# Performance work log

Hardware: AMD Instinct MI355X
Metric: run time of the kernel (lower is better)

Reference implementation:

```python
import jax, jax.numpy as jnp
import numpy as np

N = 4096
CIN = 128
COUT = 128
J = 2
SLOPE = 0.2        # LeakyReLU negative slope (GAT-style)
NEG = -9.0e15      # mask fill value from the source
ATT = J * COUT     # att_slice


def _leaky(v):
    return jnp.where(v >= 0, v, SLOPE * v)


def setup_inputs() -> dict:
    key = jax.random.key(0)
    ks = jax.random.split(key, 12)
    x = jax.random.normal(ks[0], (N, CIN), dtype=jnp.float32)

    def sparse_op(k):
        kv, km = jax.random.split(k)
        vals = jax.random.normal(kv, (N, N), dtype=jnp.float32)
        mask = jax.random.uniform(km, (N, N)) < 0.05
        return jnp.where(mask, vals, 0.0)

    Lu = sparse_op(ks[1])
    Ld = sparse_op(ks[2])
    P = jax.random.normal(ks[3], (N, N), dtype=jnp.float32) * 0.01  # harmonic projector

    s = 1.0 / np.sqrt(CIN)
    Wi_w = jax.random.uniform(ks[4], (J, CIN, COUT), minval=-s, maxval=s)
    Wi_b = jax.random.uniform(ks[5], (J, COUT), minval=-s, maxval=s)
    Ws_w = jax.random.uniform(ks[6], (J, CIN, COUT), minval=-s, maxval=s)
    Ws_b = jax.random.uniform(ks[7], (J, COUT), minval=-s, maxval=s)
    Wh_w = jax.random.uniform(ks[8], (CIN, COUT), minval=-s, maxval=s)
    Wh_b = jax.random.uniform(ks[9], (COUT,), minval=-s, maxval=s)
    att_irr = jax.random.normal(ks[10], (2 * ATT, 1), dtype=jnp.float32) * 0.1
    att_sol = jax.random.normal(ks[11], (2 * ATT, 1), dtype=jnp.float32) * 0.1
    return {"x": x, "Lu": Lu, "Ld": Ld, "P": P,
            "Wi_w": Wi_w, "Wi_b": Wi_b, "Ws_w": Ws_w, "Ws_b": Ws_b,
            "Wh_w": Wh_w, "Wh_b": Wh_b, "att_irr": att_irr, "att_sol": att_sol}


def reference(x, Lu, Ld, P, Wi_w, Wi_b, Ws_w, Ws_b, Wh_w, Wh_b, att_irr, att_sol):
    n = x.shape[0]
    # concat_j W_irr[j](x) -> [N, J*COUT] (j-major matches torch.cat along dim=1)
    x_irr = (jnp.einsum('nc,jco->njo', x, Wi_w) + Wi_b[None]).reshape(n, ATT)
    x_sol = (jnp.einsum('nc,jco->njo', x, Ws_w) + Ws_b[None]).reshape(n, ATT)

    # GAT-style scores: E[i,j] = leaky(s1[i] + s2[j])
    E_irr = _leaky(x_irr @ att_irr[:ATT] + (x_irr @ att_irr[ATT:]).T)
    E_sol = _leaky(x_sol @ att_sol[:ATT] + (x_sol @ att_sol[ATT:]).T)
    E_irr = jnp.where(Ld != 0, E_irr, NEG)
    E_sol = jnp.where(Lu != 0, E_sol, NEG)
    alpha_irr = jax.nn.softmax(E_irr, axis=1)  # dropout: eval mode -> identity
    alpha_sol = jax.nn.softmax(E_sol, axis=1)

    z = (alpha_irr @ x) @ Wi_w[0] + Wi_b[0] + (alpha_sol @ x) @ Ws_w[0] + Ws_b[0]
    for p in range(1, J):  # Laplacian-power aggregation
        alpha_irr = alpha_irr @ Ld
        alpha_sol = alpha_sol @ Lu
        z = z + (alpha_irr @ x) @ Wi_w[p] + Wi_b[p]
        z = z + (alpha_sol @ x) @ Ws_w[p] + Ws_b[p]
    z = z + (P @ x) @ Wh_w + Wh_b
    return z
```

## Files before the change

kernel.cpp:

```cpp
#include <hip/hip_runtime.h>

#define NN 4096
#define CAP 384
#define SLOPE 0.2f

typedef __attribute__((ext_vector_type(8))) short bf16x8;
typedef __attribute__((ext_vector_type(4))) float f32x4;

static __device__ __forceinline__ short f2bf(float f) {
  unsigned u = __builtin_bit_cast(unsigned, f);
  unsigned r = (u + 0x7fffu + ((u >> 16) & 1u)) >> 16;
  return (short)r;
}

#define V_OFF     0
#define C_OFF     512
#define BT_OFF    516
#define S_OFF     1024
#define HXI_OFF   32768
#define HXS_OFF   (HXI_OFF + NN*128)
#define UI_OFF    (HXS_OFF + NN*128)
#define US_OFF    (UI_OFF + NN*128)
#define XWH_OFF   (US_OFF + NN*128)
#define OI_OFF    (XWH_OFF + NN*128)
#define OS_OFF    (OI_OFF + NN*128)
#define ZP_OFF    (OS_OFF + NN*128)
#define WS_FLOATS (ZP_OFF + 8*NN*128)
#define IDX_BYTE_OFF ((size_t)WS_FLOATS * 4)
#define VAL_BYTE_OFF (IDX_BYTE_OFF + (size_t)2*NN*CAP*2)
#define CNT_BYTE_OFF (VAL_BYTE_OFF + (size_t)2*NN*CAP*4)
#define XWT_BYTE_OFF (CNT_BYTE_OFF + (size_t)2*NN*4)

__global__ __launch_bounds__(128) void k_prep(
    const float* __restrict__ Wi_w, const float* __restrict__ Wi_b,
    const float* __restrict__ Ws_w, const float* __restrict__ Ws_b,
    const float* __restrict__ Wh_b, const float* __restrict__ att_irr,
    const float* __restrict__ att_sol, float* __restrict__ ws) {
  const int t = threadIdx.x;
  float v1i = 0.f, v2i = 0.f, v1s = 0.f, v2s = 0.f;
  for (int j = 0; j < 2; ++j) {
    for (int o = 0; o < 128; ++o) {
      const float wi = Wi_w[j*16384 + t*128 + o];
      const float wv = Ws_w[j*16384 + t*128 + o];
      v1i += wi * att_irr[j*128 + o];
      v2i += wi * att_irr[256 + j*128 + o];
      v1s += wv * att_sol[j*128 + o];
      v2s += wv * att_sol[256 + j*128 + o];
    }
  }
  ws[V_OFF + t]       = v1i;
  ws[V_OFF + 128 + t] = v2i;
  ws[V_OFF + 256 + t] = v1s;
  ws[V_OFF + 384 + t] = v2s;
  ws[BT_OFF + t] = Wi_b[t] + Wi_b[128 + t] + Ws_b[t] + Ws_b[128 + t] + Wh_b[t];
  if (t < 4) {
    const float* bb = (t < 2) ? Wi_b : Ws_b;
    const float* aa = ((t < 2) ? att_irr : att_sol) + ((t & 1) ? 256 : 0);
    float c = 0.f;
    for (int k = 0; k < 256; ++k) c += bb[k] * aa[k];
    ws[C_OFF + t] = c;
  }
}

__global__ __launch_bounds__(256) void k_scores(const float* __restrict__ x,
                                                float* __restrict__ ws) {
  const int wave = threadIdx.x >> 6, lane = threadIdx.x & 63;
  const int row = blockIdx.x * 4 + wave;
  const float* v = ws + V_OFF;
  const float x0 = x[row*128 + lane];
  const float x1 = x[row*128 + 64 + lane];
  float p0 = x0 * v[lane]       + x1 * v[64 + lane];
  float p1 = x0 * v[128 + lane] + x1 * v[192 + lane];
  float p2 = x0 * v[256 + lane] + x1 * v[320 + lane];
  float p3 = x0 * v[384 + lane] + x1 * v[448 + lane];
  #pragma unroll
  for (int off = 32; off; off >>= 1) {
    p0 += __shfl_down(p0, off);
    p1 += __shfl_down(p1, off);
    p2 += __shfl_down(p2, off);
    p3 += __shfl_down(p3, off);
  }
  if (lane == 0) {
    ws[S_OFF + row]          = p0 + ws[C_OFF + 0];
    ws[S_OFF + NN + row]     = p1 + ws[C_OFF + 1];
    ws[S_OFF + 2*NN + row]   = p2 + ws[C_OFF + 2];
    ws[S_OFF + 3*NN + row]   = p3 + ws[C_OFF + 3];
  }
}

__global__ __launch_bounds__(256) void k_zero(int* __restrict__ cnt) {
  cnt[blockIdx.x * 256 + threadIdx.x] = 0;
}

__global__ __launch_bounds__(256) void k_csr(
    const float* __restrict__ Ld, const float* __restrict__ Lu,
    int* __restrict__ cntbuf, unsigned short* __restrict__ idxb,
    float* __restrict__ valb) {
  const int w = threadIdx.x >> 6, lane = threadIdx.x & 63;
  const int W = blockIdx.x * 4 + w;
  const int br = W >> 14;
  const int row = (W >> 2) & (NN - 1);
  const int quarter = W & 3;
  const float4* __restrict__ L4 =
      (const float4*)((br ? Lu : Ld) + (size_t)row * NN + quarter * 1024);
  float4 lv[4];
  #pragma unroll
  for (int i = 0; i < 4; ++i) lv[i] = L4[i*64 + lane];

  unsigned long long m[16];
  int runs[16];
  int run = 0;
  #pragma unroll
  for (int i = 0; i < 4; ++i)
    #pragma unroll
    for (int c = 0; c < 4; ++c) {
      const int r = i*4 + c;
      m[r] = __ballot((&lv[i].x)[c] != 0.f);
      runs[r] = run;
      run += (int)__popcll(m[r]);
    }
  int base = 0;
  if (lane == 0 && run) base = atomicAdd(&cntbuf[br*NN + row], run);
  base = __shfl(base, 0);
  const size_t rb = (size_t)(br*NN + row) * CAP;
  const unsigned long long lmask = (1ull << lane) - 1ull;
  #pragma unroll
  for (int i = 0; i < 4; ++i)
    #pragma unroll
    for (int c = 0; c < 4; ++c) {
      const int r = i*4 + c;
      const float v = (&lv[i].x)[c];
      if (v != 0.f) {
        const int pos = base + runs[r] + (int)__popcll(m[r] & lmask);
        if (pos < CAP) {
          idxb[rb + pos] = (unsigned short)(quarter*1024 + (i*64 + lane)*4 + c);
          valb[rb + pos] = v;
        }
      }
    }
}

__global__ __launch_bounds__(256) void k_gather_hx(
    const float* __restrict__ Ld, const float* __restrict__ Lu,
    const float* __restrict__ x, float* __restrict__ ws,
    const unsigned short* __restrict__ idxb, const float* __restrict__ valb,
    const int* __restrict__ cntbuf) {
  const int w = threadIdx.x >> 6, lane = threadIdx.x & 63;
  const int W = blockIdx.x * 4 + w;
  const int br = W >> 12;
  const int row = W & (NN - 1);
  const float2* __restrict__ x2 = (const float2*)x;
  float2* __restrict__ Hx2 = (float2*)(ws + (br ? HXS_OFF : HXI_OFF));
  const int cnt = cntbuf[br*NN + row];
  float a0 = 0.f, a1 = 0.f;
  if (cnt <= CAP) {
    const size_t rb = (size_t)(br*NN + row) * CAP;
    int jv[6]; float vv[6];
    #pragma unroll
    for (int s = 0; s < 6; ++s) {
      const int p = s*64 + lane;
      const bool in = p < cnt;
      jv[s] = in ? (int)idxb[rb + p] : 0;
      vv[s] = in ? valb[rb + p] : 0.f;
    }
    #pragma unroll
    for (int s = 0; s < 6; ++s) {
      if (s*64 < cnt) {
        const int qn = min(64, cnt - s*64);
        const int jvs = jv[s]; const float vvs = vv[s];
        int q = 0;
        for (; q + 8 <= qn; q += 8) {
          const int j0=__shfl(jvs,q+0), j1=__shfl(jvs,q+1), j2=__shfl(jvs,q+2), j3=__shfl(jvs,q+3);
          const int j4=__shfl(jvs,q+4), j5=__shfl(jvs,q+5), j6=__shfl(jvs,q+6), j7=__shfl(jvs,q+7);
          const float v0=__shfl(vvs,q+0), v1=__shfl(vvs,q+1), v2=__shfl(vvs,q+2), v3=__shfl(vvs,q+3);
          const float v4=__shfl(vvs,q+4), v5=__shfl(vvs,q+5), v6=__shfl(vvs,q+6), v7=__shfl(vvs,q+7);
          const float2 g0=x2[j0*64+lane], g1=x2[j1*64+lane], g2=x2[j2*64+lane], g3=x2[j3*64+lane];
          const float2 g4=x2[j4*64+lane], g5=x2[j5*64+lane], g6=x2[j6*64+lane], g7=x2[j7*64+lane];
          a0+=v0*g0.x; a1+=v0*g0.y; a0+=v1*g1.x; a1+=v1*g1.y;
          a0+=v2*g2.x; a1+=v2*g2.y; a0+=v3*g3.x; a1+=v3*g3.y;
          a0+=v4*g4.x; a1+=v4*g4.y; a0+=v5*g5.x; a1+=v5*g5.y;
          a0+=v6*g6.x; a1+=v6*g6.y; a0+=v7*g7.x; a1+=v7*g7.y;
        }
        for (; q < qn; ++q) {
          const int j = __shfl(jvs, q); const float v = __shfl(vvs, q);
          const float2 g = x2[j*64+lane];
          a0 += v*g.x; a1 += v*g.y;
        }
      }
    }
  } else {
    const float* __restrict__ Lrow = (br ? Lu : Ld) + (size_t)row * NN;
    for (int j = 0; j < NN; ++j) {
      const float v = Lrow[j];
      if (v != 0.f) { const float2 g = x2[j*64+lane]; a0 += v*g.x; a1 += v*g.y; }
    }
  }
  float2 o; o.x = a0; o.y = a1;
  Hx2[row*64 + lane] = o;
}

__global__ __launch_bounds__(256) void k_ugemm(
    const float* __restrict__ x, const float* __restrict__ Wi_w,
    const float* __restrict__ Ws_w, const float* __restrict__ Wh_w,
    float* __restrict__ ws) {
  const int rb = blockIdx.x;
  const int sel = blockIdx.y;
  const float* A[2]; const float* W[2]; int npass; float* out;
  if (sel == 0)      { A[0]=x; W[0]=Wi_w; A[1]=ws+HXI_OFF; W[1]=Wi_w+16384; npass=2; out=ws+UI_OFF; }
  else if (sel == 1) { A[0]=x; W[0]=Ws_w; A[1]=ws+HXS_OFF; W[1]=Ws_w+16384; npass=2; out=ws+US_OFF; }
  else               { A[0]=x; W[0]=Wh_w; A[1]=nullptr;    W[1]=nullptr;    npass=1; out=ws+XWH_OFF; }

  __shared__ __align__(16) float At[32][33];
  __shared__ __align__(16) float Wt[32][132];
  const int t = threadIdx.x;
  const int rg = t >> 4, cg = t & 15;
  const int r0 = rb * 32;
  float acc[2][8];
  #pragma unroll
  for (int i = 0; i < 2; ++i)
    #pragma unroll
    for (int j = 0; j < 8; ++j) acc[i][j] = 0.f;

  for (int ps = 0; ps < npass; ++ps) {
    const float* __restrict__ Ap = A[ps];
    const float* __restrict__ Wp = W[ps];
    for (int k0 = 0; k0 < 128; k0 += 32) {
      __syncthreads();
      { const int row = t >> 3, kq = t & 7;
        const float4 av = *(const float4*)&Ap[(r0 + row)*128 + k0 + kq*4];
        At[row][kq*4+0] = av.x; At[row][kq*4+1] = av.y;
        At[row][kq*4+2] = av.z; At[row][kq*4+3] = av.w; }
      #pragma unroll
      for (int l = 0; l < 4; ++l) {
        const int idx = t + l*256;
        const int kr = idx >> 5, c4 = idx & 31;
        const float4 wv = *(const float4*)&Wp[(k0 + kr)*128 + c4*4];
        Wt[kr][c4*4+0] = wv.x; Wt[kr][c4*4+1] = wv.y;
        Wt[kr][c4*4+2] = wv.z; Wt[kr][c4*4+3] = wv.w;
      }
      __syncthreads();
      #pragma unroll
      for (int k = 0; k < 32; ++k) {
        const float a0 = At[rg*2 + 0][k];
        const float a1 = At[rg*2 + 1][k];
        const float4 b0 = *(const float4*)&Wt[k][cg*8];
        const float4 b1 = *(const float4*)&Wt[k][cg*8 + 4];
        acc[0][0] += a0*b0.x; acc[0][1] += a0*b0.y; acc[0][2] += a0*b0.z; acc[0][3] += a0*b0.w;
        acc[0][4] += a0*b1.x; acc[0][5] += a0*b1.y; acc[0][6] += a0*b1.z; acc[0][7] += a0*b1.w;
        acc[1][0] += a1*b0.x; acc[1][1] += a1*b0.y; acc[1][2] += a1*b0.z; acc[1][3] += a1*b0.w;
        acc[1][4] += a1*b1.x; acc[1][5] += a1*b1.y; acc[1][6] += a1*b1.z; acc[1][7] += a1*b1.w;
      }
    }
  }
  #pragma unroll
  for (int i = 0; i < 2; ++i) {
    const int r = r0 + rg*2 + i;
    #pragma unroll
    for (int j = 0; j < 8; ++j) out[r*128 + cg*8 + j] = acc[i][j];
  }
}

__global__ __launch_bounds__(256) void k_xwt(const float* __restrict__ ws,
                                             unsigned short* __restrict__ XwT) {
  const float* __restrict__ Xw = ws + XWH_OFF;
  __shared__ float tile[64][133];
  const int t = threadIdx.x;
  const int k0 = blockIdx.x * 64;
  #pragma unroll
  for (int lp = 0; lp < 8; ++lp) {
    const int idx = t + lp*256;
    const int r = idx >> 5, c4 = idx & 31;
    const float4 v = *(const float4*)&Xw[(size_t)(k0 + r)*128 + c4*4];
    tile[r][c4*4+0]=v.x; tile[r][c4*4+1]=v.y; tile[r][c4*4+2]=v.z; tile[r][c4*4+3]=v.w;
  }
  __syncthreads();
  const int n = t >> 1, seg = t & 1;
  unsigned out[16];
  #pragma unroll
  for (int q = 0; q < 16; ++q) {
    const int kk = seg*32 + q*2;
    const unsigned lo = (unsigned)(unsigned short)f2bf(tile[kk][n]);
    const unsigned hi = (unsigned)(unsigned short)f2bf(tile[kk+1][n]);
    out[q] = lo | (hi << 16);
  }
  unsigned* __restrict__ dst = (unsigned*)&XwT[(size_t)n*NN + k0 + seg*32];
  #pragma unroll
  for (int q = 0; q < 16; ++q) dst[q] = out[q];
}

__global__ __launch_bounds__(256) void k_pgemm(const float* __restrict__ P,
                                               const unsigned short* __restrict__ XwT,
                                               float* __restrict__ zpart) {
  const int t = threadIdx.x;
  const int w = t >> 6, l = t & 63;
  const int quad = l >> 4, m16 = l & 15;
  const int r0 = blockIdx.x * 64;
  const int kz = blockIdx.y;
  const int row = r0 + w*16 + m16;
  const float* __restrict__ Arow = P + (size_t)row * NN;
  const int kbase = kz * 512;

  f32x4 acc[8];
  #pragma unroll
  for (int nt = 0; nt < 8; ++nt) acc[nt] = (f32x4){0.f, 0.f, 0.f, 0.f};

  float4 a0 = *(const float4*)&Arow[kbase + quad*8];
  float4 a1 = *(const float4*)&Arow[kbase + quad*8 + 4];
  for (int ks = 0; ks < 16; ++ks) {
    const int k0 = kbase + ks*32;
    bf16x8 bf[8];
    #pragma unroll
    for (int nt = 0; nt < 8; ++nt)
      bf[nt] = *(const bf16x8*)&XwT[(size_t)(nt*16 + m16) * NN + k0 + quad*8];
    float4 na0, na1;
    if (ks < 15) {
      na0 = *(const float4*)&Arow[k0 + 32 + quad*8];
      na1 = *(const float4*)&Arow[k0 + 32 + quad*8 + 4];
    }
    bf16x8 af;
    af[0]=f2bf(a0.x); af[1]=f2bf(a0.y); af[2]=f2bf(a0.z); af[3]=f2bf(a0.w);
    af[4]=f2bf(a1.x); af[5]=f2bf(a1.y); af[6]=f2bf(a1.z); af[7]=f2bf(a1.w);
    #pragma unroll
    for (int nt = 0; nt < 8; ++nt)
      acc[nt] = __builtin_amdgcn_mfma_f32_16x16x32_bf16(af, bf[nt], acc[nt], 0, 0, 0);
    a0 = na0; a1 = na1;
  }
  float* __restrict__ zp = zpart + (size_t)kz * NN * 128;
  #pragma unroll
  for (int nt = 0; nt < 8; ++nt)
    #pragma unroll
    for (int r = 0; r < 4; ++r)
      zp[(size_t)(r0 + w*16 + quad*4 + r)*128 + nt*16 + m16] = acc[nt][r];
}

__global__ __launch_bounds__(256) void k_attn(
    const float* __restrict__ Ld, const float* __restrict__ Lu,
    float* __restrict__ ws, const unsigned short* __restrict__ idxb,
    const int* __restrict__ cntbuf) {
  const int w = threadIdx.x >> 6, lane = threadIdx.x & 63;
  const int W = blockIdx.x * 4 + w;
  const int br = W >> 12;
  const int row = W & (NN - 1);
  const float2* __restrict__ U2 = (const float2*)(ws + (br ? US_OFF : UI_OFF));
  float2* __restrict__ O2 = (float2*)(ws + (br ? OS_OFF : OI_OFF));
  const float s1 = ws[S_OFF + (br ? 2*NN : 0) + row];
  const float* __restrict__ s2a = ws + S_OFF + (br ? 3*NN : NN);
  const int cnt = cntbuf[br*NN + row];
  float a0 = 0.f, a1 = 0.f;
  float den = 0.f;

  if (cnt > 0 && cnt <= CAP) {
    const size_t rb = (size_t)(br*NN + row) * CAP;
    int jv[6]; float ev[6];
    float dl = 0.f;
    #pragma unroll
    for (int s = 0; s < 6; ++s) {
      const int p = s*64 + lane;
      if (p < cnt) {
        const int j = (int)idxb[rb + p];
        const float sc = s1 + s2a[j];
        const float e = expf(sc >= 0.f ? sc : SLOPE * sc);
        jv[s] = j; ev[s] = e; dl += e;
      } else { jv[s] = 0; ev[s] = 0.f; }
    }
    #pragma unroll
    for (int off = 32; off; off >>= 1) dl += __shfl_xor(dl, off);
    den = dl;
    #pragma unroll
    for (int s = 0; s < 6; ++s) {
      if (s*64 < cnt) {
        const int qn = min(64, cnt - s*64);
        const int jvs = jv[s]; const float evs = ev[s];
        int q = 0;
        for (; q + 8 <= qn; q += 8) {
          const int j0=__shfl(jvs,q+0), j1=__shfl(jvs,q+1), j2=__shfl(jvs,q+2), j3=__shfl(jvs,q+3);
          const int j4=__shfl(jvs,q+4), j5=__shfl(jvs,q+5), j6=__shfl(jvs,q+6), j7=__shfl(jvs,q+7);
          const float e0=__shfl(evs,q+0), e1=__shfl(evs,q+1), e2=__shfl(evs,q+2), e3=__shfl(evs,q+3);
          const float e4=__shfl(evs,q+4), e5=__shfl(evs,q+5), e6=__shfl(evs,q+6), e7=__shfl(evs,q+7);
          const float2 g0=U2[j0*64+lane], g1=U2[j1*64+lane], g2=U2[j2*64+lane], g3=U2[j3*64+lane];
          const float2 g4=U2[j4*64+lane], g5=U2[j5*64+lane], g6=U2[j6*64+lane], g7=U2[j7*64+lane];
          a0+=e0*g0.x; a1+=e0*g0.y; a0+=e1*g1.x; a1+=e1*g1.y;
          a0+=e2*g2.x; a1+=e2*g2.y; a0+=e3*g3.x; a1+=e3*g3.y;
          a0+=e4*g4.x; a1+=e4*g4.y; a0+=e5*g5.x; a1+=e5*g5.y;
          a0+=e6*g6.x; a1+=e6*g6.y; a0+=e7*g7.x; a1+=e7*g7.y;
        }
        for (; q < qn; ++q) {
          const int j = __shfl(jvs, q); const float e = __shfl(evs, q);
          const float2 g = U2[j*64+lane];
          a0 += e*g.x; a1 += e*g.y;
        }
      }
    }
    float2 o; o.x = a0 / den; o.y = a1 / den;
    O2[row*64 + lane] = o;
  } else if (cnt == 0) {
    for (int j = 0; j < NN; ++j) { const float2 g = U2[j*64+lane]; a0 += g.x; a1 += g.y; }
    float2 o; o.x = a0 * (1.f/NN); o.y = a1 * (1.f/NN);
    O2[row*64 + lane] = o;
  } else {
    const float* __restrict__ Lrow = (br ? Lu : Ld) + (size_t)row * NN;
    for (int j = 0; j < NN; ++j) {
      const float v = Lrow[j];
      if (v != 0.f) {
        const float sc = s1 + s2a[j];
        const float e = expf(sc >= 0.f ? sc : SLOPE * sc);
        const float2 g = U2[j*64+lane];
        a0 += e*g.x; a1 += e*g.y; den += e;
      }
    }
    float2 o; o.x = a0 / den; o.y = a1 / den;
    O2[row*64 + lane] = o;
  }
}

__global__ __launch_bounds__(256) void k_combine(const float* __restrict__ ws,
                                                 float* __restrict__ z) {
  const int i = blockIdx.x * 256 + threadIdx.x;
  const int col = i & 127;
  float acc = ws[BT_OFF + col] + ws[OI_OFF + i] + ws[OS_OFF + i];
  #pragma unroll
  for (int kz = 0; kz < 8; ++kz) acc += ws[ZP_OFF + kz*NN*128 + i];
  z[i] = acc;
}

extern "C" void kernel_launch(void* const* d_in, const int* in_sizes, int n_in,
                              void* d_out, int out_size, void* d_ws, size_t ws_size,
                              hipStream_t stream) {
  const float* x       = (const float*)d_in[0];
  const float* Lu      = (const float*)d_in[1];
  const float* Ld      = (const float*)d_in[2];
  const float* P       = (const float*)d_in[3];
  const float* Wi_w    = (const float*)d_in[4];
  const float* Wi_b    = (const float*)d_in[5];
  const float* Ws_w    = (const float*)d_in[6];
  const float* Ws_b    = (const float*)d_in[7];
  const float* Wh_w    = (const float*)d_in[8];
  const float* Wh_b    = (const float*)d_in[9];
  const float* att_irr = (const float*)d_in[10];
  const float* att_sol = (const float*)d_in[11];
  float* z  = (float*)d_out;
  float* ws = (float*)d_ws;
  unsigned short* idxb = (unsigned short*)((char*)d_ws + IDX_BYTE_OFF);
  float*          valb = (float*)((char*)d_ws + VAL_BYTE_OFF);
  int*            cntb = (int*)((char*)d_ws + CNT_BYTE_OFF);
  unsigned short* xwtb = (unsigned short*)((char*)d_ws + XWT_BYTE_OFF);

  k_prep<<<1, 128, 0, stream>>>(Wi_w, Wi_b, Ws_w, Ws_b, Wh_b, att_irr, att_sol, ws);
  k_scores<<<1024, 256, 0, stream>>>(x, ws);
  k_zero<<<32, 256, 0, stream>>>(cntb);
  k_csr<<<8192, 256, 0, stream>>>(Ld, Lu, cntb, idxb, valb);
  k_gather_hx<<<2048, 256, 0, stream>>>(Ld, Lu, x, ws, idxb, valb, cntb);
  {
    dim3 g(128, 3);
    k_ugemm<<<g, 256, 0, stream>>>(x, Wi_w, Ws_w, Wh_w, ws);
  }
  k_xwt<<<64, 256, 0, stream>>>(ws, xwtb);
  {
    dim3 g(64, 8);
    k_pgemm<<<g, 256, 0, stream>>>(P, xwtb, ws + ZP_OFF);
  }
  k_attn<<<2048, 256, 0, stream>>>(Ld, Lu, ws, idxb, cntb);
  k_combine<<<NN * 128 / 256, 256, 0, stream>>>(ws, z);
}
```

Before: 410.8 us.

## Split-bf16 P GEMM, precompute attention exps in CSR build, simplify gathers

The P@(xWh) GEMM now represents both operands as bf16 high and low halves and issues three MFMAs per tile (hi*hi, lo*hi, hi*lo) to recover near-fp32 accuracy, which triples the MFMA work and doubles the B-operand loads. The CSR builder now also computes the exponentiated attention score per nonzero and stores column indices as 32-bit, so k_attn no longer recomputes exp or reads s2. The gather loops drop the shuffle-broadcast scheme and use uniform scalar loads of indices and values, with wave-uniform row ids via readfirstlane. CAP drops from 384 to 288, so rows with more nonzeros take the slow dense fallback more often.

Result: slower. 444.8 us (+8.3%).

```diff
diff --git a/kernel.cpp b/kernel.cpp
--- a/kernel.cpp
+++ b/kernel.cpp
@@ -1,16 +1,18 @@
 #include <hip/hip_runtime.h>
 
 #define NN 4096
-#define CAP 384
+#define CAP 288
 #define SLOPE 0.2f
 
 typedef __attribute__((ext_vector_type(8))) short bf16x8;
 typedef __attribute__((ext_vector_type(4))) float f32x4;
 
-static __device__ __forceinline__ short f2bf(float f) {
+static __device__ __forceinline__ unsigned f2bf(float f) {
   unsigned u = __builtin_bit_cast(unsigned, f);
-  unsigned r = (u + 0x7fffu + ((u >> 16) & 1u)) >> 16;
-  return (short)r;
+  return (u + 0x7fffu + ((u >> 16) & 1u)) >> 16;
+}
+static __device__ __forceinline__ float bf2f(unsigned h) {
+  return __builtin_bit_cast(float, h << 16);
 }
 
 #define V_OFF     0
@@ -26,10 +28,12 @@
 #define OS_OFF    (OI_OFF + NN*128)
 #define ZP_OFF    (OS_OFF + NN*128)
 #define WS_FLOATS (ZP_OFF + 8*NN*128)
-#define IDX_BYTE_OFF ((size_t)WS_FLOATS * 4)
-#define VAL_BYTE_OFF (IDX_BYTE_OFF + (size_t)2*NN*CAP*2)
-#define CNT_BYTE_OFF (VAL_BYTE_OFF + (size_t)2*NN*CAP*4)
-#define XWT_BYTE_OFF (CNT_BYTE_OFF + (size_t)2*NN*4)
+#define JB_BYTE_OFF  ((size_t)WS_FLOATS * 4)
+#define VB_BYTE_OFF  (JB_BYTE_OFF  + (size_t)2*NN*CAP*4)
+#define EB_BYTE_OFF  (VB_BYTE_OFF  + (size_t)2*NN*CAP*4)
+#define CNT_BYTE_OFF (EB_BYTE_OFF  + (size_t)2*NN*CAP*4)
+#define XWTH_BYTE_OFF (CNT_BYTE_OFF + (size_t)2*NN*4)
+#define XWTL_BYTE_OFF (XWTH_BYTE_OFF + (size_t)128*NN*2)
 
 __global__ __launch_bounds__(128) void k_prep(
     const float* __restrict__ Wi_w, const float* __restrict__ Wi_b,
@@ -94,15 +98,18 @@
 
 __global__ __launch_bounds__(256) void k_csr(
     const float* __restrict__ Ld, const float* __restrict__ Lu,
-    int* __restrict__ cntbuf, unsigned short* __restrict__ idxb,
-    float* __restrict__ valb) {
-  const int w = threadIdx.x >> 6, lane = threadIdx.x & 63;
-  const int W = blockIdx.x * 4 + w;
+    const float* __restrict__ ws, int* __restrict__ cntbuf,
+    unsigned* __restrict__ jbuf, float* __restrict__ valb,
+    float* __restrict__ eb) {
+  const int lane = threadIdx.x & 63;
+  const int W = __builtin_amdgcn_readfirstlane(blockIdx.x * 4 + (threadIdx.x >> 6));
   const int br = W >> 14;
   const int row = (W >> 2) & (NN - 1);
   const int quarter = W & 3;
   const float4* __restrict__ L4 =
       (const float4*)((br ? Lu : Ld) + (size_t)row * NN + quarter * 1024);
+  const float s1 = ws[S_OFF + (br ? 2*NN : 0) + row];
+  const float* __restrict__ s2a = ws + S_OFF + (br ? 3*NN : NN);
   float4 lv[4];
   #pragma unroll
   for (int i = 0; i < 4; ++i) lv[i] = L4[i*64 + lane];
@@ -133,8 +140,11 @@
       if (v != 0.f) {
         const int pos = base + runs[r] + (int)__popcll(m[r] & lmask);
         if (pos < CAP) {
-          idxb[rb + pos] = (unsigned short)(quarter*1024 + (i*64 + lane)*4 + c);
+          const int jj = quarter*1024 + (i*64 + lane)*4 + c;
+          jbuf[rb + pos] = (unsigned)jj;
           valb[rb + pos] = v;
+          const float sc = s1 + s2a[jj];
+          eb[rb + pos] = expf(sc >= 0.f ? sc : SLOPE * sc);
         }
       }
     }
@@ -143,10 +153,10 @@
 __global__ __launch_bounds__(256) void k_gather_hx(
     const float* __restrict__ Ld, const float* __restrict__ Lu,
     const float* __restrict__ x, float* __restrict__ ws,
-    const unsigned short* __restrict__ idxb, const float* __restrict__ valb,
+    const unsigned* __restrict__ jbuf, const float* __restrict__ valb,
     const int* __restrict__ cntbuf) {
-  const int w = threadIdx.x >> 6, lane = threadIdx.x & 63;
-  const int W = blockIdx.x * 4 + w;
+  const int lane = threadIdx.x & 63;
+  const int W = __builtin_amdgcn_readfirstlane(blockIdx.x * 4 + (threadIdx.x >> 6));
   const int br = W >> 12;
   const int row = W & (NN - 1);
   const float2* __restrict__ x2 = (const float2*)x;
@@ -154,45 +164,27 @@
   const int cnt = cntbuf[br*NN + row];
   float a0 = 0.f, a1 = 0.f;
   if (cnt <= CAP) {
-    const size_t rb = (size_t)(br*NN + row) * CAP;
-    int jv[6]; float vv[6];
-    #pragma unroll
-    for (int s = 0; s < 6; ++s) {
-      const int p = s*64 + lane;
-      const bool in = p < cnt;
-      jv[s] = in ? (int)idxb[rb + p] : 0;
-      vv[s] = in ? valb[rb + p] : 0.f;
-    }
-    #pragma unroll
-    for (int s = 0; s < 6; ++s) {
-      if (s*64 < cnt) {
-        const int qn = min(64, cnt - s*64);
-        const int jvs = jv[s]; const float vvs = vv[s];
-        int q = 0;
-        for (; q + 8 <= qn; q += 8) {
-          const int j0=__shfl(jvs,q+0), j1=__shfl(jvs,q+1), j2=__shfl(jvs,q+2), j3=__shfl(jvs,q+3);
-          const int j4=__shfl(jvs,q+4), j5=__shfl(jvs,q+5), j6=__shfl(jvs,q+6), j7=__shfl(jvs,q+7);
-          const float v0=__shfl(vvs,q+0), v1=__shfl(vvs,q+1), v2=__shfl(vvs,q+2), v3=__shfl(vvs,q+3);
-          const float v4=__shfl(vvs,q+4), v5=__shfl(vvs,q+5), v6=__shfl(vvs,q+6), v7=__shfl(vvs,q+7);
-          const float2 g0=x2[j0*64+lane], g1=x2[j1*64+lane], g2=x2[j2*64+lane], g3=x2[j3*64+lane];
-          const float2 g4=x2[j4*64+lane], g5=x2[j5*64+lane], g6=x2[j6*64+lane], g7=x2[j7*64+lane];
-          a0+=v0*g0.x; a1+=v0*g0.y; a0+=v1*g1.x; a1+=v1*g1.y;
-          a0+=v2*g2.x; a1+=v2*g2.y; a0+=v3*g3.x; a1+=v3*g3.y;
-          a0+=v4*g4.x; a1+=v4*g4.y; a0+=v5*g5.x; a1+=v5*g5.y;
-          a0+=v6*g6.x; a1+=v6*g6.y; a0+=v7*g7.x; a1+=v7*g7.y;
-        }
-        for (; q < qn; ++q) {
-          const int j = __shfl(jvs, q); const float v = __shfl(vvs, q);
-          const float2 g = x2[j*64+lane];
-          a0 += v*g.x; a1 += v*g.y;
-        }
-      }
+    const unsigned* __restrict__ jb = jbuf + (size_t)(br*NN + row) * CAP;
+    const float* __restrict__ vb = valb + (size_t)(br*NN + row) * CAP;
+    int p = 0;
+    for (; p + 8 <= cnt; p += 8) {
+      unsigned j[8]; float wv[8]; float2 g[8];
+      #pragma unroll
+      for (int i = 0; i < 8; ++i) { j[i] = jb[p+i]; wv[i] = vb[p+i]; }
+      #pragma unroll
+      for (int i = 0; i < 8; ++i) g[i] = x2[(size_t)j[i]*64 + lane];
+      #pragma unroll
+      for (int i = 0; i < 8; ++i) { a0 += wv[i]*g[i].x; a1 += wv[i]*g[i].y; }
+    }
+    for (; p < cnt; ++p) {
+      const float2 g = x2[(size_t)jb[p]*64 + lane];
+      a0 += vb[p]*g.x; a1 += vb[p]*g.y;
     }
   } else {
     const float* __restrict__ Lrow = (br ? Lu : Ld) + (size_t)row * NN;
     for (int j = 0; j < NN; ++j) {
       const float v = Lrow[j];
-      if (v != 0.f) { const float2 g = x2[j*64+lane]; a0 += v*g.x; a1 += v*g.y; }
+      if (v != 0.f) { const float2 g = x2[(size_t)j*64 + lane]; a0 += v*g.x; a1 += v*g.y; }
     }
   }
   float2 o; o.x = a0; o.y = a1;
@@ -261,7 +253,8 @@
 }
 
 __global__ __launch_bounds__(256) void k_xwt(const float* __restrict__ ws,
-                                             unsigned short* __restrict__ XwT) {
+                                             unsigned short* __restrict__ XwTh,
+                                             unsigned short* __restrict__ XwTl) {
   const float* __restrict__ Xw = ws + XWH_OFF;
   __shared__ float tile[64][133];
   const int t = threadIdx.x;
@@ -275,21 +268,25 @@
   }
   __syncthreads();
   const int n = t >> 1, seg = t & 1;
-  unsigned out[16];
+  unsigned oh[16], ol[16];
   #pragma unroll
   for (int q = 0; q < 16; ++q) {
     const int kk = seg*32 + q*2;
-    const unsigned lo = (unsigned)(unsigned short)f2bf(tile[kk][n]);
-    const unsigned hi = (unsigned)(unsigned short)f2bf(tile[kk+1][n]);
-    out[q] = lo | (hi << 16);
-  }
-  unsigned* __restrict__ dst = (unsigned*)&XwT[(size_t)n*NN + k0 + seg*32];
-  #pragma unroll
-  for (int q = 0; q < 16; ++q) dst[q] = out[q];
+    const float f0 = tile[kk][n], f1 = tile[kk+1][n];
+    const unsigned h0 = f2bf(f0), h1 = f2bf(f1);
+    const unsigned l0 = f2bf(f0 - bf2f(h0)), l1 = f2bf(f1 - bf2f(h1));
+    oh[q] = h0 | (h1 << 16);
+    ol[q] = l0 | (l1 << 16);
+  }
+  unsigned* __restrict__ dh = (unsigned*)&XwTh[(size_t)n*NN + k0 + seg*32];
+  unsigned* __restrict__ dl = (unsigned*)&XwTl[(size_t)n*NN + k0 + seg*32];
+  #pragma unroll
+  for (int q = 0; q < 16; ++q) { dh[q] = oh[q]; dl[q] = ol[q]; }
 }
 
 __global__ __launch_bounds__(256) void k_pgemm(const float* __restrict__ P,
-                                               const unsigned short* __restrict__ XwT,
+                                               const unsigned short* __restrict__ XwTh,
+                                               const unsigned short* __restrict__ XwTl,
                                                float* __restrict__ zpart) {
   const int t = threadIdx.x;
   const int w = t >> 6, l = t & 63;
@@ -308,21 +305,35 @@
   float4 a1 = *(const float4*)&Arow[kbase + quad*8 + 4];
   for (int ks = 0; ks < 16; ++ks) {
     const int k0 = kbase + ks*32;
-    bf16x8 bf[8];
-    #pragma unroll
-    for (int nt = 0; nt < 8; ++nt)
-      bf[nt] = *(const bf16x8*)&XwT[(size_t)(nt*16 + m16) * NN + k0 + quad*8];
+    bf16x8 bh[8], bl[8];
+    #pragma unroll
+    for (int nt = 0; nt < 8; ++nt) {
+      bh[nt] = *(const bf16x8*)&XwTh[(size_t)(nt*16 + m16) * NN + k0 + quad*8];
+      bl[nt] = *(const bf16x8*)&XwTl[(size_t)(nt*16 + m16) * NN + k0 + quad*8];
+    }
     float4 na0, na1;
     if (ks < 15) {
       na0 = *(const float4*)&Arow[k0 + 32 + quad*8];
       na1 = *(const float4*)&Arow[k0 + 32 + quad*8 + 4];
     }
-    bf16x8 af;
-    af[0]=f2bf(a0.x); af[1]=f2bf(a0.y); af[2]=f2bf(a0.z); af[3]=f2bf(a0.w);
-    af[4]=f2bf(a1.x); af[5]=f2bf(a1.y); af[6]=f2bf(a1.z); af[7]=f2bf(a1.w);
+    bf16x8 ah, al;
+    #pragma unroll
+    for (int c = 0; c < 4; ++c) {
+      const float f0 = (&a0.x)[c], f1 = (&a1.x)[c];
+      const unsigned h0 = f2bf(f0), h1 = f2bf(f1);
+      ah[c]   = (short)h0; ah[c+4] = (short)h1;
+      al[c]   = (short)f2bf(f0 - bf2f(h0));
+      al[c+4] = (short)f2bf(f1 - bf2f(h1));
+    }
     #pragma unroll
     for (int nt = 0; nt < 8; ++nt)
-      acc[nt] = __builtin_amdgcn_mfma_f32_16x16x32_bf16(af, bf[nt], acc[nt], 0, 0, 0);
+      acc[nt] = __builtin_amdgcn_mfma_f32_16x16x32_bf16(ah, bh[nt], acc[nt], 0, 0, 0);
+    #pragma unroll
+    for (int nt = 0; nt < 8; ++nt)
+      acc[nt] = __builtin_amdgcn_mfma_f32_16x16x32_bf16(al, bh[nt], acc[nt], 0, 0, 0);
+    #pragma unroll
+    for (int nt = 0; nt < 8; ++nt)
+      acc[nt] = __builtin_amdgcn_mfma_f32_16x16x32_bf16(ah, bl[nt], acc[nt], 0, 0, 0);
     a0 = na0; a1 = na1;
   }
   float* __restrict__ zp = zpart + (size_t)kz * NN * 128;
@@ -335,76 +346,50 @@
 
 __global__ __launch_bounds__(256) void k_attn(
     const float* __restrict__ Ld, const float* __restrict__ Lu,
-    float* __restrict__ ws, const unsigned short* __restrict__ idxb,
-    const int* __restrict__ cntbuf) {
-  const int w = threadIdx.x >> 6, lane = threadIdx.x & 63;
-  const int W = blockIdx.x * 4 + w;
+    float* __restrict__ ws, const unsigned* __restrict__ jbuf,
+    const float* __restrict__ eb, const int* __restrict__ cntbuf) {
+  const int lane = threadIdx.x & 63;
+  const int W = __builtin_amdgcn_readfirstlane(blockIdx.x * 4 + (threadIdx.x >> 6));
   const int br = W >> 12;
   const int row = W & (NN - 1);
   const float2* __restrict__ U2 = (const float2*)(ws + (br ? US_OFF : UI_OFF));
   float2* __restrict__ O2 = (float2*)(ws + (br ? OS_OFF : OI_OFF));
-  const float s1 = ws[S_OFF + (br ? 2*NN : 0) + row];
-  const float* __restrict__ s2a = ws + S_OFF + (br ? 3*NN : NN);
   const int cnt = cntbuf[br*NN + row];
-  float a0 = 0.f, a1 = 0.f;
-  float den = 0.f;
+  float a0 = 0.f, a1 = 0.f, den = 0.f;
 
   if (cnt > 0 && cnt <= CAP) {
-    const size_t rb = (size_t)(br*NN + row) * CAP;
-    int jv[6]; float ev[6];
-    float dl = 0.f;
-    #pragma unroll
-    for (int s = 0; s < 6; ++s) {
-      const int p = s*64 + lane;
-      if (p < cnt) {
-        const int j = (int)idxb[rb + p];
-        const float sc = s1 + s2a[j];
-        const float e = expf(sc >= 0.f ? sc : SLOPE * sc);
-        jv[s] = j; ev[s] = e; dl += e;
-      } else { jv[s] = 0; ev[s] = 0.f; }
-    }
-    #pragma unroll
-    for (int off = 32; off; off >>= 1) dl += __shfl_xor(dl, off);
-    den = dl;
-    #pragma unroll
-    for (int s = 0; s < 6; ++s) {
-      if (s*64 < cnt) {
-        const int qn = min(64, cnt - s*64);
-        const int jvs = jv[s]; const float evs = ev[s];
-        int q = 0;
-        for (; q + 8 <= qn; q += 8) {
-          const int j0=__shfl(jvs,q+0), j1=__shfl(jvs,q+1), j2=__shfl(jvs,q+2), j3=__shfl(jvs,q+3);
-          const int j4=__shfl(jvs,q+4), j5=__shfl(jvs,q+5), j6=__shfl(jvs,q+6), j7=__shfl(jvs,q+7);
-          const float e0=__shfl(evs,q+0), e1=__shfl(evs,q+1), e2=__shfl(evs,q+2), e3=__shfl(evs,q+3);
-          const float e4=__shfl(evs,q+4), e5=__shfl(evs,q+5), e6=__shfl(evs,q+6), e7=__shfl(evs,q+7);
-          const float2 g0=U2[j0*64+lane], g1=U2[j1*64+lane], g2=U2[j2*64+lane], g3=U2[j3*64+lane];
-          const float2 g4=U2[j4*64+lane], g5=U2[j5*64+lane], g6=U2[j6*64+lane], g7=U2[j7*64+lane];
-          a0+=e0*g0.x; a1+=e0*g0.y; a0+=e1*g1.x; a1+=e1*g1.y;
-          a0+=e2*g2.x; a1+=e2*g2.y; a0+=e3*g3.x; a1+=e3*g3.y;
-          a0+=e4*g4.x; a1+=e4*g4.y; a0+=e5*g5.x; a1+=e5*g5.y;
-          a0+=e6*g6.x; a1+=e6*g6.y; a0+=e7*g7.x; a1+=e7*g7.y;
-        }
-        for (; q < qn; ++q) {
-          const int j = __shfl(jvs, q); const float e = __shfl(evs, q);
-          const float2 g = U2[j*64+lane];
-          a0 += e*g.x; a1 += e*g.y;
-        }
-      }
+    const unsigned* __restrict__ jb = jbuf + (size_t)(br*NN + row) * CAP;
+    const float* __restrict__ el = eb + (size_t)(br*NN + row) * CAP;
+    int p = 0;
+    for (; p + 8 <= cnt; p += 8) {
+      unsigned j[8]; float e[8]; float2 g[8];
+      #pragma unroll
+      for (int i = 0; i < 8; ++i) { j[i] = jb[p+i]; e[i] = el[p+i]; }
+      #pragma unroll
+      for (int i = 0; i < 8; ++i) g[i] = U2[(size_t)j[i]*64 + lane];
+      #pragma unroll
+      for (int i = 0; i < 8; ++i) { a0 += e[i]*g[i].x; a1 += e[i]*g[i].y; den += e[i]; }
+    }
+    for (; p < cnt; ++p) {
+      const float2 g = U2[(size_t)jb[p]*64 + lane];
+      a0 += el[p]*g.x; a1 += el[p]*g.y; den += el[p];
     }
     float2 o; o.x = a0 / den; o.y = a1 / den;
     O2[row*64 + lane] = o;
   } else if (cnt == 0) {
-    for (int j = 0; j < NN; ++j) { const float2 g = U2[j*64+lane]; a0 += g.x; a1 += g.y; }
+    for (int j = 0; j < NN; ++j) { const float2 g = U2[(size_t)j*64 + lane]; a0 += g.x; a1 += g.y; }
     float2 o; o.x = a0 * (1.f/NN); o.y = a1 * (1.f/NN);
     O2[row*64 + lane] = o;
   } else {
+    const float s1 = ws[S_OFF + (br ? 2*NN : 0) + row];
+    const float* __restrict__ s2a = ws + S_OFF + (br ? 3*NN : NN);
     const float* __restrict__ Lrow = (br ? Lu : Ld) + (size_t)row * NN;
     for (int j = 0; j < NN; ++j) {
       const float v = Lrow[j];
       if (v != 0.f) {
         const float sc = s1 + s2a[j];
         const float e = expf(sc >= 0.f ? sc : SLOPE * sc);
-        const float2 g = U2[j*64+lane];
+        const float2 g = U2[(size_t)j*64 + lane];
         a0 += e*g.x; a1 += e*g.y; den += e;
       }
     }
@@ -440,25 +425,27 @@
   const float* att_sol = (const float*)d_in[11];
   float* z  = (float*)d_out;
   float* ws = (float*)d_ws;
-  unsigned short* idxb = (unsigned short*)((char*)d_ws + IDX_BYTE_OFF);
-  float*          valb = (float*)((char*)d_ws + VAL_BYTE_OFF);
+  unsigned*       jbuf = (unsigned*)((char*)d_ws + JB_BYTE_OFF);
+  float*          valb = (float*)((char*)d_ws + VB_BYTE_OFF);
+  float*          ebuf = (float*)((char*)d_ws + EB_BYTE_OFF);
   int*            cntb = (int*)((char*)d_ws + CNT_BYTE_OFF);
-  unsigned short* xwtb = (unsigned short*)((char*)d_ws + XWT_BYTE_OFF);
+  unsigned short* xwth = (unsigned short*)((char*)d_ws + XWTH_BYTE_OFF);
+  unsigned short* xwtl = (unsigned short*)((char*)d_ws + XWTL_BYTE_OFF);
 
   k_prep<<<1, 128, 0, stream>>>(Wi_w, Wi_b, Ws_w, Ws_b, Wh_b, att_irr, att_sol, ws);
   k_scores<<<1024, 256, 0, stream>>>(x, ws);
   k_zero<<<32, 256, 0, stream>>>(cntb);
-  k_csr<<<8192, 256, 0, stream>>>(Ld, Lu, cntb, idxb, valb);
-  k_gather_hx<<<2048, 256, 0, stream>>>(Ld, Lu, x, ws, idxb, valb, cntb);
+  k_csr<<<8192, 256, 0, stream>>>(Ld, Lu, ws, cntb, jbuf, valb, ebuf);
+  k_gather_hx<<<2048, 256, 0, stream>>>(Ld, Lu, x, ws, jbuf, valb, cntb);
   {
     dim3 g(128, 3);
     k_ugemm<<<g, 256, 0, stream>>>(x, Wi_w, Ws_w, Wh_w, ws);
   }
-  k_xwt<<<64, 256, 0, stream>>>(ws, xwtb);
+  k_xwt<<<64, 256, 0, stream>>>(ws, xwth, xwtl);
   {
     dim3 g(64, 8);
-    k_pgemm<<<g, 256, 0, stream>>>(P, xwtb, ws + ZP_OFF);
-  }
-  k_attn<<<2048, 256, 0, stream>>>(Ld, Lu, ws, idxb, cntb);
+    k_pgemm<<<g, 256, 0, stream>>>(P, xwth, xwtl, ws + ZP_OFF);
+  }
+  k_attn<<<2048, 256, 0, stream>>>(Ld, Lu, ws, jbuf, ebuf, cntb);
   k_combine<<<NN * 128 / 256, 256, 0, stream>>>(ws, z);
 }
```
